# Kernel tuning notes

Measured on AMD Instinct MI355X. Metric: run time of the kernel, lower is better.

## Reference

```python
import jax, jax.numpy as jnp
import numpy as np

N_NODES, N_EDGES, HID = 30000, 480000, 128
N_GRAPHS, N_CLASSES = 128, 6
BN_EPS, ADD_SCORE = 1e-5, 0.5


def setup_inputs():
    key = jax.random.key(0)
    ks = jax.random.split(key, 12)
    g = lambda i, shape: jax.random.normal(ks[i], shape, jnp.float32) * 0.05
    return dict(
        x=jax.random.normal(ks[0], (N_NODES, HID), jnp.float32),
        edge_index=jax.random.randint(ks[1], (2, N_EDGES), 0, N_NODES, jnp.int32),
        batch=jnp.sort(jax.random.randint(ks[2], (N_NODES,), 0, N_GRAPHS, jnp.int32)),
        Wl=g(3, (6, HID, HID)), bl=jnp.zeros((6, HID), jnp.float32),
        Wr=g(4, (6, HID, HID)),
        gamma=jnp.ones((6, HID), jnp.float32), beta=jnp.zeros((6, HID), jnp.float32),
        Wlin=g(5, (3, HID, 2 * HID)), blin=jnp.zeros((3, HID), jnp.float32),
        Wp=g(6, (3, 2 * HID)), bp=jnp.zeros((3,), jnp.float32),
        Wf1=g(7, (HID, HID)), bf1=jnp.zeros((HID,), jnp.float32),
        Wf2=g(8, (N_CLASSES, HID)), bf2=jnp.zeros((N_CLASSES,), jnp.float32),
    )


def _sage(x, src, dst, emf, Wl_i, bl_i, Wr_i, N):
    # PyG SAGEConv: lin_l(mean_{j->i} x_j) + lin_r(x_i); emf masks dead edges
    msg = x[src] * emf[:, None]                              # [E,H]
    s = jax.ops.segment_sum(msg, dst, num_segments=N)
    c = jax.ops.segment_sum(emf, dst, num_segments=N)
    mean = s / jnp.maximum(c, 1.0)[:, None]
    return mean @ Wl_i.T + bl_i + x @ Wr_i.T


def _bn(x, g, b, nvf):
    # training-mode BatchNorm over valid (non-merged-away) nodes only
    cnt = jnp.maximum(nvf.sum(), 1.0)
    mu = (x * nvf[:, None]).sum(0) / cnt
    var = (((x - mu) ** 2) * nvf[:, None]).sum(0) / cnt
    return g * (x - mu) * jax.lax.rsqrt(var + BN_EPS) + b


def _edge_pool(x, src, dst, emb, nvb, Wp_i, bp_i, N, E):
    h = x.shape[1]
    # raw edge score = Linear(cat(x[src], x[dst]))
    raw = (x @ Wp_i[:h])[src] + (x @ Wp_i[h:])[dst] + bp_i   # [E]
    neg = jnp.finfo(x.dtype).min
    mx = jax.ops.segment_max(jnp.where(emb, raw, neg), dst, num_segments=N)
    z = jnp.where(emb, jnp.exp(jnp.where(emb, raw - mx[dst], 0.0)), 0.0)
    den = jax.ops.segment_sum(z, dst, num_segments=N)
    score = z / jnp.maximum(den, 1e-16)[dst] + ADD_SCORE     # softmax per dst + 0.5

    # greedy edge matching in descending score order (sequential, int-only carry)
    order = jnp.argsort(-jnp.where(emb, jax.lax.stop_gradient(score), -jnp.inf))

    def step(carry, i):
        matched, cluster, chosen = carry
        s, t = src[i], dst[i]
        ok = emb[i] & (~matched[s]) & (~matched[t]) & (s != t)
        rep, oth = jnp.minimum(s, t), jnp.maximum(s, t)
        matched = matched.at[s].set(matched[s] | ok)
        matched = matched.at[t].set(matched[t] | ok)
        cluster = cluster.at[oth].set(jnp.where(ok, rep, cluster[oth]))
        chosen = chosen.at[rep].set(jnp.where(ok, i, chosen[rep]))
        return (matched, cluster, chosen), None

    init = (~nvb, jnp.arange(N, dtype=jnp.int32), jnp.full((N,), -1, jnp.int32))
    (matched, cluster, chosen), _ = jax.lax.scan(step, init, order)

    # merged node = (x_s + x_t) * score(chosen edge); singleton score = 1
    nscore = jnp.where(chosen >= 0, score[jnp.maximum(chosen, 0)], 1.0)
    new_x = jax.ops.segment_sum(x, cluster, num_segments=N) * nscore[:, None]
    nvb2 = nvb & (cluster == jnp.arange(N, dtype=jnp.int32))
    # remap edges to cluster representatives; coalesce duplicates (self-loops kept, as PyG)
    key = jnp.where(emb, cluster[src] * N + cluster[dst], -1)  # N*N < 2**31
    uk = jnp.unique(key, size=E, fill_value=-1)
    emb2 = uk >= 0
    ukc = jnp.maximum(uk, 0)
    return new_x, ukc // N, ukc % N, emb2, nvb2


def reference(x, edge_index, batch, Wl, bl, Wr, gamma, beta, Wlin, blin, Wp, bp, Wf1, bf1, Wf2, bf2):
    N, E = x.shape[0], edge_index.shape[1]
    src, dst = edge_index[0], edge_index[1]
    emb = jnp.ones((E,), bool)   # edge-valid mask (fixed-shape graph coarsening)
    nvb = jnp.ones((N,), bool)   # node-valid mask
    for blk in range(3):
        emf, nvf = emb.astype(x.dtype), nvb.astype(x.dtype)
        i = 2 * blk
        h = _bn(jax.nn.relu(_sage(x, src, dst, emf, Wl[i], bl[i], Wr[i], N)), gamma[i], beta[i], nvf)
        h2 = _bn(jax.nn.relu(_sage(h, src, dst, emf, Wl[i + 1], bl[i + 1], Wr[i + 1], N)), gamma[i + 1], beta[i + 1], nvf)
        x = jnp.concatenate([h2, h], axis=1) @ Wlin[blk].T + blin[blk]  # dropout = identity (eval)
        x, src, dst, emb, nvb = _edge_pool(x, src, dst, emb, nvb, Wp[blk], bp[blk], N, E)
    nvf = nvb.astype(x.dtype)
    sums = jax.ops.segment_sum(x * nvf[:, None], batch, num_segments=N_GRAPHS)
    cnt = jax.ops.segment_sum(nvf, batch, num_segments=N_GRAPHS)
    pooled = sums / jnp.maximum(cnt, 1.0)[:, None]           # global_mean_pool
    hfc = jax.nn.relu(pooled @ Wf1.T + bf1)
    return jax.nn.log_softmax(hfc @ Wf2.T + bf2, axis=1)
```

## Files before the change

### kernel.cpp

```cpp
#include <hip/hip_runtime.h>
#include <stdint.h>

#define NN 30000
#define NE 480000
#define HID 128
#define NG 128
#define NC 6
#define BN_EPS 1e-5f
#define WPB 938
#define SLOTS 4

typedef unsigned int u32;
typedef unsigned long long u64;

__global__ void k_init(const int* __restrict__ ei, int* srcA, int* dstA, int* nvb,
                       int* scal, int* b3, int* i2, float* gbuf) {
  int t = blockIdx.x * 256 + threadIdx.x;
  if (t < NE) { srcA[t] = ei[t]; dstA[t] = ei[NE + t]; }
  if (t < NN) nvb[t] = 1;
  if (t < 2 * NN) { b3[t] = 0; i2[t] = 0; }
  if (t < NG * HID + NG) gbuf[t] = 0.f;
  if (t == 0) { scal[0] = NE; scal[1] = 0; }
}

__global__ void k_csr_count(const int* __restrict__ pE, const int* __restrict__ src,
                            const int* __restrict__ dst, int* __restrict__ cnt,
                            int* __restrict__ icnt, const int* __restrict__ nvb,
                            int* __restrict__ pcnt) {
  int t = blockIdx.x * 256 + threadIdx.x;
  if (t < NN && nvb[t]) atomicAdd(pcnt, 1);
  if (t < *pE) {
    int s = src[t], d = dst[t];
    atomicAdd(&cnt[d], 1);
    if (s != d) { atomicAdd(&icnt[s], 1); atomicAdd(&icnt[d], 1); }
  }
}

__global__ __launch_bounds__(1024) void k_scan2(const int* __restrict__ in0, int* __restrict__ out0,
                                                const int* __restrict__ in1, int* __restrict__ out1) {
  const int* in = blockIdx.x ? in1 : in0;
  int* out = blockIdx.x ? out1 : out0;
  __shared__ int part[1024];
  int t = threadIdx.x;
  int chunk = (NN + 1023) / 1024;
  int b = t * chunk, e = b + chunk;
  if (b > NN) b = NN;
  if (e > NN) e = NN;
  int s = 0;
  for (int i = b; i < e; i++) s += in[i];
  part[t] = s;
  __syncthreads();
  for (int off = 1; off < 1024; off <<= 1) {
    int v = (t >= off) ? part[t - off] : 0;
    __syncthreads();
    part[t] += v;
    __syncthreads();
  }
  int excl = (t == 0) ? 0 : part[t - 1];
  for (int i = b; i < e; i++) { out[i] = excl; excl += in[i]; }
  if (t == 0) out[NN] = part[1023];
}

__global__ void k_csr_scatter(const int* __restrict__ pE, const int* __restrict__ src,
                              const int* __restrict__ dst, const int* __restrict__ coff,
                              int* __restrict__ cursor, int* __restrict__ eids,
                              const int* __restrict__ ioff, int* __restrict__ icur,
                              int* __restrict__ ieids) {
  int e = blockIdx.x * 256 + threadIdx.x;
  if (e >= *pE) return;
  int s = src[e], d = dst[e];
  int pos = coff[d] + atomicAdd(&cursor[d], 1);
  eids[pos] = e;
  if (s != d) {
    int p1 = ioff[s] + atomicAdd(&icur[s], 1); ieids[p1] = e;
    int p2 = ioff[d] + atomicAdd(&icur[d], 1); ieids[p2] = e;
  }
}

__global__ __launch_bounds__(256) void k_sage_gather(
    const int* __restrict__ coff, const int* __restrict__ eids,
    const int* __restrict__ src, const float* __restrict__ x,
    float* __restrict__ mean) {
  int grp = threadIdx.x >> 5;
  int lane = threadIdx.x & 31;
  int n = blockIdx.x * 8 + grp;
  if (n >= NN) return;
  int b = coff[n], e2 = coff[n + 1];
  float4 acc = make_float4(0.f, 0.f, 0.f, 0.f);
  for (int i = b; i < e2; i++) {
    int s = src[eids[i]];
    float4 v = *(const float4*)(x + (size_t)s * HID + lane * 4);
    acc.x += v.x; acc.y += v.y; acc.z += v.z; acc.w += v.w;
  }
  float inv = 1.0f / fmaxf((float)(e2 - b), 1.0f);
  acc.x *= inv; acc.y *= inv; acc.z *= inv; acc.w *= inv;
  *(float4*)(mean + (size_t)n * HID + lane * 4) = acc;
}

__global__ __launch_bounds__(256) void gemm_dual(
    const float* __restrict__ A1, const float* __restrict__ W1,
    const float* __restrict__ A2, const float* __restrict__ W2,
    const float* __restrict__ bias, float* __restrict__ out,
    int M, int ldw, int relu, double* __restrict__ bnsum) {
  if (blockIdx.x == 0 && threadIdx.x < 2 * HID) bnsum[threadIdx.x] = 0.0;
  __shared__ float As[64][33];
  __shared__ float Ws[32][132];
  int row0 = blockIdx.x * 64;
  int tid = threadIdx.x;
  int cid = tid & 31;
  int rid = tid >> 5;
  float acc[8][4];
#pragma unroll
  for (int r = 0; r < 8; r++)
#pragma unroll
    for (int c = 0; c < 4; c++) acc[r][c] = 0.f;

  for (int srcI = 0; srcI < 2; ++srcI) {
    const float* A = srcI ? A2 : A1;
    const float* W = srcI ? W2 : W1;
    for (int kc = 0; kc < 128; kc += 32) {
#pragma unroll
      for (int i = 0; i < 2; ++i) {
        int idx = tid + i * 256;
        int r = idx >> 3;
        int c4 = (idx & 7) << 2;
        int gr = row0 + r;
        float4 v = make_float4(0.f, 0.f, 0.f, 0.f);
        if (gr < M) v = *(const float4*)(A + (size_t)gr * 128 + kc + c4);
        As[r][c4 + 0] = v.x; As[r][c4 + 1] = v.y; As[r][c4 + 2] = v.z; As[r][c4 + 3] = v.w;
      }
#pragma unroll
      for (int i = 0; i < 4; ++i) {
        int idx = tid + i * 256;
        int j = idx >> 3;
        int c4 = (idx & 7) << 2;
        float4 v = *(const float4*)(W + (size_t)j * ldw + kc + c4);
        Ws[c4 + 0][j] = v.x; Ws[c4 + 1][j] = v.y; Ws[c4 + 2][j] = v.z; Ws[c4 + 3][j] = v.w;
      }
      __syncthreads();
#pragma unroll
      for (int kk = 0; kk < 32; ++kk) {
        float4 w = *(const float4*)(&Ws[kk][cid * 4]);
#pragma unroll
        for (int r = 0; r < 8; ++r) {
          float a = As[rid * 8 + r][kk];
          acc[r][0] += a * w.x; acc[r][1] += a * w.y; acc[r][2] += a * w.z; acc[r][3] += a * w.w;
        }
      }
      __syncthreads();
    }
  }
#pragma unroll
  for (int r = 0; r < 8; ++r) {
    int gr = row0 + rid * 8 + r;
    if (gr >= M) continue;
#pragma unroll
    for (int c = 0; c < 4; ++c) {
      float v = acc[r][c] + bias[cid * 4 + c];
      if (relu) v = fmaxf(v, 0.f);
      out[(size_t)gr * 128 + cid * 4 + c] = v;
    }
  }
}

__global__ __launch_bounds__(128) void k_bn_stats(const float* __restrict__ x,
                                                  const int* __restrict__ nvb,
                                                  double* __restrict__ sums) {
  int k = threadIdx.x;
  int n0 = blockIdx.x * 64;
  float s = 0.f, q = 0.f;
  for (int r = 0; r < 64; r++) {
    int n = n0 + r;
    if (n >= NN) break;
    if (!nvb[n]) continue;
    float v = x[(size_t)n * HID + k];
    s += v; q += v * v;
  }
  atomicAdd(&sums[k], (double)s);
  atomicAdd(&sums[HID + k], (double)q);
}

__global__ void k_bn_apply(float* __restrict__ x, const double* __restrict__ sums,
                           const int* __restrict__ cnt, const float* __restrict__ gamma,
                           const float* __restrict__ beta) {
  int t = blockIdx.x * 256 + threadIdx.x;
  if (t >= NN * HID) return;
  int k = t & 127;
  double c = (double)((*cnt > 1) ? *cnt : 1);
  double mu = sums[k] / c;
  double var = sums[HID + k] / c - mu * mu;
  if (var < 0.0) var = 0.0;
  float inv = (float)(1.0 / sqrt(var + (double)BN_EPS));
  x[t] = gamma[k] * (x[t] - (float)mu) * inv + beta[k];
}

__global__ void k_node_proj(const float* __restrict__ x, const float* __restrict__ Wp,
                            float* __restrict__ px1, float* __restrict__ px2) {
  int n = blockIdx.x * 256 + threadIdx.x;
  if (n >= NN) return;
  const float* xr = x + (size_t)n * HID;
  float s1 = 0.f, s2 = 0.f;
#pragma unroll 8
  for (int k = 0; k < HID; k += 4) {
    float4 v = *(const float4*)(xr + k);
    float4 w1 = *(const float4*)(Wp + k);
    float4 w2 = *(const float4*)(Wp + HID + k);
    s1 += v.x * w1.x + v.y * w1.y + v.z * w1.z + v.w * w1.w;
    s2 += v.x * w2.x + v.y * w2.y + v.z * w2.z + v.w * w2.w;
  }
  px1[n] = s1; px2[n] = s2;
}

__global__ void k_edge_softmax_seed(
    const int* __restrict__ coff, const int* __restrict__ eids,
    const int* __restrict__ src, const float* __restrict__ px1,
    const float* __restrict__ px2, const float* __restrict__ bp,
    float* __restrict__ score, u64* __restrict__ ekey, u64* __restrict__ S) {
  int n = blockIdx.x * 256 + threadIdx.x;
  if (n >= NN) return;
  S[n] = 0ull;
  int b = coff[n], e2 = coff[n + 1];
  if (b == e2) return;
  float p2 = px2[n] + *bp;
  float mx = -3.4e38f;
  for (int i = b; i < e2; i++) {
    float r = px1[src[eids[i]]] + p2;
    mx = fmaxf(mx, r);
  }
  double den = 0.0;
  for (int i = b; i < e2; i++) {
    int eid = eids[i];
    float z = expf(px1[src[eid]] + p2 - mx);
    score[eid] = z;
    den += (double)z;
  }
  if (den < 1e-16) den = 1e-16;
  double invd = 1.0 / den;
  for (int i = b; i < e2; i++) {
    int eid = eids[i];
    float sc = (float)((double)score[eid] * invd) + 0.5f;
    score[eid] = sc;
    ekey[eid] = ((u64)__float_as_uint(sc) << 32) | (u64)(0xFFFFFFFFu - (u32)eid);
  }
}

__global__ __launch_bounds__(256) void k_suitor(
    const int* __restrict__ ioff, const int* __restrict__ ieids,
    const int* __restrict__ src, const int* __restrict__ dst,
    const u64* __restrict__ ekey, u64* __restrict__ S) {
  int wid = threadIdx.x >> 6;
  int lane = threadIdx.x & 63;
  int n = blockIdx.x * 4 + wid;
  if (n >= NN) return;
  int cur = n;
  while (cur >= 0) {
    int b = ioff[cur], e2 = ioff[cur + 1];
    int deg = e2 - b;
    if (deg == 0) break;
    if (deg <= 64 * SLOTS) {
      u64 key[SLOTS]; int pv[SLOTS];
#pragma unroll
      for (int s = 0; s < SLOTS; s++) {
        key[s] = 0; pv[s] = 0;
        int i = b + s * 64 + lane;
        if (i < e2) {
          int e = ieids[i];
          key[s] = ekey[e];
          int es = src[e], ed = dst[e];
          pv[s] = (es == cur) ? ed : es;
        }
      }
      long long res;
      for (;;) {
        u64 localBest = 0;
#pragma unroll
        for (int s = 0; s < SLOTS; s++) {
          if (!key[s]) continue;
          u64 sv = __hip_atomic_load(&S[pv[s]], __ATOMIC_RELAXED, __HIP_MEMORY_SCOPE_AGENT);
          if (sv >= key[s]) key[s] = 0;
          else if (key[s] > localBest) localBest = key[s];
        }
        u64 bestKey = localBest;
#pragma unroll
        for (int o = 32; o > 0; o >>= 1) {
          u64 other = __shfl_xor(bestKey, o, 64);
          if (other > bestKey) bestKey = other;
        }
        if (bestKey == 0) { res = -1; break; }
        int ms = -1;
#pragma unroll
        for (int s = 0; s < SLOTS; s++)
          if (ms < 0 && key[s] == bestKey) ms = s;
        u64 ball = __ballot(ms >= 0);
        int owner = (int)(__ffsll((long long)ball) - 1);
        long long r0 = -3;
        if (lane == owner) {
          int bv = pv[ms];
          u64 old = atomicMax(&S[bv], bestKey);
          if (old >= bestKey) { key[ms] = 0; r0 = -2; }
          else if (old == 0) r0 = -1;
          else {
            int eo = (int)(0xFFFFFFFFu - (u32)(old & 0xFFFFFFFFull));
            int so = src[eo], do_ = dst[eo];
            r0 = (so == bv) ? do_ : so;
          }
        }
        res = __shfl(r0, owner, 64);
        if (res != -2) break;
      }
      if (res < 0) break;
      cur = (int)res;
    } else {
      u64 bestKey = 0;
      for (int i = b + lane; i < e2; i += 64) {
        int e = ieids[i];
        u64 k = ekey[e];
        if (k <= bestKey) continue;
        int es = src[e], ed = dst[e];
        int v = (es == cur) ? ed : es;
        u64 sv = __hip_atomic_load(&S[v], __ATOMIC_RELAXED, __HIP_MEMORY_SCOPE_AGENT);
        if (k > sv) bestKey = k;
      }
#pragma unroll
      for (int o = 32; o > 0; o >>= 1) {
        u64 other = __shfl_xor(bestKey, o, 64);
        if (other > bestKey) bestKey = other;
      }
      long long r0 = -1;
      if (bestKey != 0 && lane == 0) {
        int e = (int)(0xFFFFFFFFu - (u32)(bestKey & 0xFFFFFFFFull));
        int es = src[e], ed = dst[e];
        int bv = (es == cur) ? ed : es;
        u64 old = atomicMax(&S[bv], bestKey);
        if (old >= bestKey) r0 = cur;
        else if (old != 0) {
          int eo = (int)(0xFFFFFFFFu - (u32)(old & 0xFFFFFFFFull));
          int so = src[eo], do_ = dst[eo];
          r0 = (so == bv) ? do_ : so;
        }
      }
      long long res = (bestKey != 0) ? __shfl(r0, 0, 64) : -1;
      cur = (int)res;
    }
  }
}

__global__ __launch_bounds__(256) void k_new_x(
    const u64* __restrict__ S, const int* __restrict__ src, const int* __restrict__ dst,
    const float* __restrict__ score, const float* __restrict__ x,
    float* __restrict__ out, int* __restrict__ cluster,
    int* __restrict__ nvb, int* __restrict__ b3zero) {
  int gt = blockIdx.x * 256 + threadIdx.x;
  if (gt < 2 * NN) b3zero[gt] = 0;
  int grp = threadIdx.x >> 5;
  int lane = threadIdx.x & 31;
  int n = blockIdx.x * 8 + grp;
  if (n >= NN) return;
  u64 k = S[n];
  int partner = -1;
  bool isOth = false;
  float sc = 1.f;
  if (k) {
    int e = (int)(0xFFFFFFFFu - (u32)(k & 0xFFFFFFFFull));
    int s = src[e], d = dst[e];
    int other = (s == n) ? d : s;
    if (S[other] == k) {
      if (n > other) isOth = true;
      else { partner = other; sc = score[e]; }
    }
  }
  float4 v = make_float4(0.f, 0.f, 0.f, 0.f);
  if (!isOth) {
    v = *(const float4*)(x + (size_t)n * HID + lane * 4);
    if (partner >= 0) {
      float4 w = *(const float4*)(x + (size_t)partner * HID + lane * 4);
      v.x = (v.x + w.x) * sc; v.y = (v.y + w.y) * sc;
      v.z = (v.z + w.z) * sc; v.w = (v.w + w.w) * sc;
    }
  }
  *(float4*)(out + (size_t)n * HID + lane * 4) = v;
  if (lane == 0) {
    int e2 = (int)(0xFFFFFFFFu - (u32)(k & 0xFFFFFFFFull));
    int s2 = isOth ? src[e2] : n;
    int d2 = isOth ? dst[e2] : n;
    cluster[n] = isOth ? (s2 < d2 ? s2 : d2) : n;
    nvb[n] = (nvb[n] && !isOth) ? 1 : 0;
  }
}

__global__ void k_bucket_count(const int* __restrict__ pE, const int* __restrict__ src,
                               const int* __restrict__ cluster, int* __restrict__ bcount) {
  int e = blockIdx.x * 256 + threadIdx.x;
  if (e >= *pE) return;
  atomicAdd(&bcount[cluster[src[e]]], 1);
}

__global__ __launch_bounds__(1024) void k_scan(const int* __restrict__ in, int* __restrict__ out,
                                               int n, int* totalDst) {
  __shared__ int part[1024];
  int t = threadIdx.x;
  int chunk = (n + 1023) / 1024;
  int b = t * chunk, e = b + chunk;
  if (b > n) b = n;
  if (e > n) e = n;
  int s = 0;
  for (int i = b; i < e; i++) s += in[i];
  part[t] = s;
  __syncthreads();
  for (int off = 1; off < 1024; off <<= 1) {
    int v = (t >= off) ? part[t - off] : 0;
    __syncthreads();
    part[t] += v;
    __syncthreads();
  }
  int excl = (t == 0) ? 0 : part[t - 1];
  int total = part[1023];
  for (int i = b; i < e; i++) { out[i] = excl; excl += in[i]; }
  if (t == 0) {
    out[n] = total;
    if (totalDst) *totalDst = total;
  }
}

__global__ void k_bucket_scatter(const int* __restrict__ pE, const int* __restrict__ src,
                                 const int* __restrict__ dst, const int* __restrict__ cluster,
                                 const int* __restrict__ boffs, int* __restrict__ bcursor,
                                 int* __restrict__ bucket) {
  int e = blockIdx.x * 256 + threadIdx.x;
  if (e >= *pE) return;
  int cs = cluster[src[e]], cd = cluster[dst[e]];
  int pos = boffs[cs] + atomicAdd(&bcursor[cs], 1);
  bucket[pos] = cd;
}

__global__ __launch_bounds__(256) void k_dedup_bitmap(
    const int* __restrict__ boffs, int* __restrict__ bucket,
    int* __restrict__ ucount) {
  __shared__ u32 bm[4][960];
  int wid = threadIdx.x >> 6;
  int lane = threadIdx.x & 63;
  int n = blockIdx.x * 4 + wid;
  int b = boffs[n], e = boffs[n + 1];
  for (int w = lane; w < 960; w += 64) bm[wid][w] = 0;
  __syncthreads();
  for (int i = b + lane; i < e; i += 64)
    atomicOr(&bm[wid][bucket[i] >> 5], 1u << (bucket[i] & 31));
  __syncthreads();
  int w0 = lane * 15;
  int w1 = w0 + 15; if (w1 > WPB) w1 = WPB;
  int cnt = 0;
  for (int w = w0; w < w1; w++) cnt += __popc(bm[wid][w]);
  int inc = cnt;
  for (int o = 1; o < 64; o <<= 1) { int v = __shfl_up(inc, o); if (lane >= o) inc += v; }
  int excl = inc - cnt;
  int total = __shfl(inc, 63);
  int pos = b + excl;
  for (int w = w0; w < w1; w++) {
    u32 v = bm[wid][w];
    while (v) { int bit = __ffs(v) - 1; bucket[pos++] = (w << 5) | bit; v &= v - 1; }
  }
  if (lane == 0) ucount[n] = total;
}

__global__ void k_emit(const int* __restrict__ boffs, const int* __restrict__ bucket,
                       const int* __restrict__ bucount, const int* __restrict__ bnoffs,
                       int* __restrict__ srcO, int* __restrict__ dstO,
                       int* __restrict__ b3zero, int* __restrict__ i2zero,
                       int* __restrict__ pcnt) {
  int t = blockIdx.x * 256 + threadIdx.x;
  int stride = gridDim.x * 256;
  for (int z = t; z < 2 * NN; z += stride) { b3zero[z] = 0; i2zero[z] = 0; }
  if (t == 0) *pcnt = 0;
  if (t >= NN) return;
  int u = bucount[t], b = boffs[t], o = bnoffs[t];
  for (int i = 0; i < u; i++) { srcO[o + i] = t; dstO[o + i] = bucket[b + i]; }
}

__global__ void k_graph_pool(const int* __restrict__ nvb, const int* __restrict__ batch,
                             const float* __restrict__ x, float* __restrict__ gsum,
                             float* __restrict__ gcnt) {
  int t = blockIdx.x * 256 + threadIdx.x;
  int n = t >> 2;
  if (n >= NN) return;
  if (!nvb[n]) return;
  int sub = t & 3;
  int g = batch[n];
  const float* xr = x + (size_t)n * HID + sub * 32;
  float* o = gsum + (size_t)g * HID + sub * 32;
#pragma unroll
  for (int i = 0; i < 8; i++) {
    float4 v = *(const float4*)(xr + i * 4);
    atomicAdd(o + i * 4 + 0, v.x); atomicAdd(o + i * 4 + 1, v.y);
    atomicAdd(o + i * 4 + 2, v.z); atomicAdd(o + i * 4 + 3, v.w);
  }
  if (sub == 0) atomicAdd(&gcnt[g], 1.0f);
}

__global__ __launch_bounds__(128) void k_head1(const float* __restrict__ gsum,
                                               const float* __restrict__ gcnt,
                                               const float* __restrict__ Wf1,
                                               const float* __restrict__ bf1,
                                               float* __restrict__ hfc) {
  int g = blockIdx.x;
  int j = threadIdx.x;
  __shared__ float p[HID];
  float c = fmaxf(gcnt[g], 1.f);
  p[j] = gsum[g * HID + j] / c;
  __syncthreads();
  float s = bf1[j];
  const float* w = Wf1 + (size_t)j * HID;
  for (int k = 0; k < HID; k++) s += p[k] * w[k];
  hfc[g * HID + j] = fmaxf(s, 0.f);
}

__global__ void k_head2(const float* __restrict__ hfc, const float* __restrict__ Wf2,
                        const float* __restrict__ bf2, float* __restrict__ out) {
  int g = blockIdx.x;
  int t = threadIdx.x;
  __shared__ float lg[NC];
  if (t < NC) {
    float s = bf2[t];
    const float* w = Wf2 + (size_t)t * HID;
    const float* h = hfc + (size_t)g * HID;
    for (int k = 0; k < HID; k++) s += h[k] * w[k];
    lg[t] = s;
  }
  __syncthreads();
  if (t == 0) {
    float m = lg[0];
    for (int c = 1; c < NC; c++) m = fmaxf(m, lg[c]);
    float se = 0.f;
    for (int c = 0; c < NC; c++) se += expf(lg[c] - m);
    float lse = m + logf(se);
    for (int c = 0; c < NC; c++) out[g * NC + c] = lg[c] - lse;
  }
}

extern "C" void kernel_launch(void* const* d_in, const int* in_sizes, int n_in,
                              void* d_out, int out_size, void* d_ws, size_t ws_size,
                              hipStream_t stream) {
  const float* x0 = (const float*)d_in[0];
  const int* ei = (const int*)d_in[1];
  const int* batch = (const int*)d_in[2];
  const float* Wl = (const float*)d_in[3];
  const float* bl = (const float*)d_in[4];
  const float* Wr = (const float*)d_in[5];
  const float* gamma = (const float*)d_in[6];
  const float* beta = (const float*)d_in[7];
  const float* Wlin = (const float*)d_in[8];
  const float* blin = (const float*)d_in[9];
  const float* Wp = (const float*)d_in[10];
  const float* bp = (const float*)d_in[11];
  const float* Wf1 = (const float*)d_in[12];
  const float* bf1 = (const float*)d_in[13];
  const float* Wf2 = (const float*)d_in[14];
  const float* bf2 = (const float*)d_in[15];
  float* out = (float*)d_out;

  const int NH = NN * HID;
  size_t off = 0;
  char* base = (char*)d_ws;
  auto carve = [&](size_t bytes) -> char* {
    char* p = base + off;
    off += (bytes + 255) & ~(size_t)255;
    return p;
  };
  float* xa = (float*)carve((size_t)NH * 4);
  float* xb = (float*)carve((size_t)NH * 4);
  float* xc = (float*)carve((size_t)NH * 4);
  float* xd = (float*)carve((size_t)NH * 4);
  int* srcA = (int*)carve((size_t)NE * 4);
  int* dstA = (int*)carve((size_t)NE * 4);
  int* srcB = (int*)carve((size_t)NE * 4);
  int* dstB = (int*)carve((size_t)NE * 4);
  float* escore = (float*)carve((size_t)NE * 4);
  int* ebucket = (int*)carve((size_t)NE * 4);
  int* eids = (int*)carve((size_t)NE * 4);
  u64* ekey = (u64*)carve((size_t)NE * 8);
  int* ieids = (int*)carve((size_t)2 * NE * 4);
  u64* S = (u64*)carve((size_t)NN * 8);
  float* npx1 = (float*)carve((size_t)NN * 4);
  float* npx2 = (float*)carve((size_t)NN * 4);
  int* ncluster = (int*)carve((size_t)NN * 4);
  int* nvb = (int*)carve((size_t)NN * 4);
  int* b3 = (int*)carve((size_t)3 * NN * 4);
  int* bcount = b3;
  int* bcursor = b3 + NN;
  int* bucount = b3 + 2 * NN;
  int* i2 = (int*)carve((size_t)2 * NN * 4);
  int* icnt = i2;
  int* icursor = i2 + NN;
  int* boffs = (int*)carve((size_t)(NN + 1) * 4);
  int* bnoffs = (int*)carve((size_t)(NN + 1) * 4);
  int* csroff = (int*)carve((size_t)(NN + 1) * 4);
  int* ioff = (int*)carve((size_t)(NN + 1) * 4);
  double* bnsum = (double*)carve((size_t)2 * HID * 8);
  float* gbuf = (float*)carve((size_t)(NG * HID + NG) * 4);
  float* gsum = gbuf;
  float* gcnt = gbuf + NG * HID;
  float* ghfc = (float*)carve((size_t)NG * HID * 4);
  int* scal = (int*)carve(64 * 4);
  (void)ws_size; (void)n_in; (void)in_sizes; (void)out_size;

  int* pE = scal;
  int* pcnt = scal + 1;

  hipMemcpyAsync(xa, x0, (size_t)NH * 4, hipMemcpyDeviceToDevice, stream);
  k_init<<<1875, 256, 0, stream>>>(ei, srcA, dstA, nvb, scal, b3, i2, gbuf);

  int* srcC = srcA; int* dstC = dstA; int* srcN = srcB; int* dstN = dstB;
  float* xcur = xa;
  float* xtmp = xd;

  auto sage = [&](const float* xin, float* xout, int L) {
    k_sage_gather<<<3750, 256, 0, stream>>>(csroff, eids, srcC, xin, xtmp);
    gemm_dual<<<469, 256, 0, stream>>>(xtmp, Wl + (size_t)L * HID * HID, xin,
                                       Wr + (size_t)L * HID * HID, bl + (size_t)L * HID,
                                       xout, NN, HID, 1, bnsum);
    k_bn_stats<<<469, 128, 0, stream>>>(xout, nvb, bnsum);
    k_bn_apply<<<15000, 256, 0, stream>>>(xout, bnsum, pcnt, gamma + (size_t)L * HID,
                                          beta + (size_t)L * HID);
  };

  for (int b = 0; b < 3; b++) {
    k_csr_count<<<1875, 256, 0, stream>>>(pE, srcC, dstC, bcount, icnt, nvb, pcnt);
    k_scan2<<<2, 1024, 0, stream>>>(bcount, csroff, icnt, ioff);
    k_csr_scatter<<<1875, 256, 0, stream>>>(pE, srcC, dstC, csroff, bcursor, eids,
                                            ioff, icursor, ieids);

    sage(xcur, xb, 2 * b);
    sage(xb, xc, 2 * b + 1);
    gemm_dual<<<469, 256, 0, stream>>>(xc, Wlin + (size_t)b * HID * 2 * HID, xb,
                                       Wlin + (size_t)b * HID * 2 * HID + HID,
                                       blin + (size_t)b * HID, xcur, NN, 2 * HID, 0, bnsum);

    k_node_proj<<<118, 256, 0, stream>>>(xcur, Wp + (size_t)b * 2 * HID, npx1, npx2);
    k_edge_softmax_seed<<<118, 256, 0, stream>>>(csroff, eids, srcC, npx1, npx2, bp + b,
                                                 escore, ekey, S);
    k_suitor<<<7500, 256, 0, stream>>>(ioff, ieids, srcC, dstC, ekey, S);
    k_new_x<<<3750, 256, 0, stream>>>(S, srcC, dstC, escore, xcur, xtmp,
                                      ncluster, nvb, b3);

    if (b < 2) {
      k_bucket_count<<<1875, 256, 0, stream>>>(pE, srcC, ncluster, bcount);
      k_scan<<<1, 1024, 0, stream>>>(bcount, boffs, NN, (int*)nullptr);
      k_bucket_scatter<<<1875, 256, 0, stream>>>(pE, srcC, dstC, ncluster, boffs, bcursor,
                                                 ebucket);
      k_dedup_bitmap<<<7500, 256, 0, stream>>>(boffs, ebucket, bucount);
      k_scan<<<1, 1024, 0, stream>>>(bucount, bnoffs, NN, pE);
      k_emit<<<235, 256, 0, stream>>>(boffs, ebucket, bucount, bnoffs, srcN, dstN,
                                      b3, i2, pcnt);
      { int* t = srcC; srcC = srcN; srcN = t; t = dstC; dstC = dstN; dstN = t; }
    }
    { float* t = xcur; xcur = xtmp; xtmp = t; }
  }

  k_graph_pool<<<469, 256, 0, stream>>>(nvb, batch, xcur, gsum, gcnt);
  k_head1<<<NG, 128, 0, stream>>>(gsum, gcnt, Wf1, bf1, ghfc);
  k_head2<<<NG, 32, 0, stream>>>(ghfc, Wf2, bf2, out);
}
```

Measured before the change: 3.008 ms.

## Pack incidence lists with key and neighbor for suitor matching

Instead of storing edge ids in the incidence list and chasing ekey/src/dst through indirection in the suitor loop, a new scatter kernel runs after scoring and writes int4 entries holding the 64-bit key and the neighbor id. The suitor kernel then reads one contiguous 16-byte entry per incident edge, which removes the dependent random gathers from its inner loop. The list reuses the xc buffer as scratch, which is free at that point. It costs an extra kernel launch and larger per-entry writes. k_new_x also takes the cluster id directly from the partner, dropping a redundant edge lookup.

```diff
diff --git a/kernel.cpp b/kernel.cpp
--- a/kernel.cpp
+++ b/kernel.cpp
@@ -12,6 +12,10 @@
 
 typedef unsigned int u32;
 typedef unsigned long long u64;
+
+__device__ __forceinline__ u64 ent_key(int4 ent) {
+  return ((u64)(u32)ent.y << 32) | (u32)ent.x;
+}
 
 __global__ void k_init(const int* __restrict__ ei, int* srcA, int* dstA, int* nvb,
                        int* scal, int* b3, int* i2, float* gbuf) {
@@ -61,20 +65,14 @@
   if (t == 0) out[NN] = part[1023];
 }
 
-__global__ void k_csr_scatter(const int* __restrict__ pE, const int* __restrict__ src,
-                              const int* __restrict__ dst, const int* __restrict__ coff,
-                              int* __restrict__ cursor, int* __restrict__ eids,
-                              const int* __restrict__ ioff, int* __restrict__ icur,
-                              int* __restrict__ ieids) {
+__global__ void k_csr_scatter(const int* __restrict__ pE, const int* __restrict__ dst,
+                              const int* __restrict__ coff, int* __restrict__ cursor,
+                              int* __restrict__ eids) {
   int e = blockIdx.x * 256 + threadIdx.x;
   if (e >= *pE) return;
-  int s = src[e], d = dst[e];
+  int d = dst[e];
   int pos = coff[d] + atomicAdd(&cursor[d], 1);
   eids[pos] = e;
-  if (s != d) {
-    int p1 = ioff[s] + atomicAdd(&icur[s], 1); ieids[p1] = e;
-    int p2 = ioff[d] + atomicAdd(&icur[d], 1); ieids[p2] = e;
-  }
 }
 
 __global__ __launch_bounds__(256) void k_sage_gather(
@@ -244,10 +242,29 @@
   }
 }
 
+__global__ void k_inc_scatter(const int* __restrict__ pE, const int* __restrict__ src,
+                              const int* __restrict__ dst, const u64* __restrict__ ekey,
+                              const int* __restrict__ ioff, int* __restrict__ icur,
+                              int4* __restrict__ ielist) {
+  int e = blockIdx.x * 256 + threadIdx.x;
+  if (e >= *pE) return;
+  int s = src[e], d = dst[e];
+  if (s == d) return;
+  u64 k = ekey[e];
+  int4 ent;
+  ent.x = (int)(u32)(k & 0xFFFFFFFFull);
+  ent.y = (int)(u32)(k >> 32);
+  ent.w = 0;
+  ent.z = d;
+  ielist[ioff[s] + atomicAdd(&icur[s], 1)] = ent;
+  ent.z = s;
+  ielist[ioff[d] + atomicAdd(&icur[d], 1)] = ent;
+}
+
 __global__ __launch_bounds__(256) void k_suitor(
-    const int* __restrict__ ioff, const int* __restrict__ ieids,
+    const int* __restrict__ ioff, const int4* __restrict__ ielist,
     const int* __restrict__ src, const int* __restrict__ dst,
-    const u64* __restrict__ ekey, u64* __restrict__ S) {
+    u64* __restrict__ S) {
   int wid = threadIdx.x >> 6;
   int lane = threadIdx.x & 63;
   int n = blockIdx.x * 4 + wid;
@@ -264,10 +281,9 @@
         key[s] = 0; pv[s] = 0;
         int i = b + s * 64 + lane;
         if (i < e2) {
-          int e = ieids[i];
-          key[s] = ekey[e];
-          int es = src[e], ed = dst[e];
-          pv[s] = (es == cur) ? ed : es;
+          int4 ent = ielist[i];
+          key[s] = ent_key(ent);
+          pv[s] = ent.z;
         }
       }
       long long res;
@@ -313,12 +329,10 @@
     } else {
       u64 bestKey = 0;
       for (int i = b + lane; i < e2; i += 64) {
-        int e = ieids[i];
-        u64 k = ekey[e];
+        int4 ent = ielist[i];
+        u64 k = ent_key(ent);
         if (k <= bestKey) continue;
-        int es = src[e], ed = dst[e];
-        int v = (es == cur) ? ed : es;
-        u64 sv = __hip_atomic_load(&S[v], __ATOMIC_RELAXED, __HIP_MEMORY_SCOPE_AGENT);
+        u64 sv = __hip_atomic_load(&S[ent.z], __ATOMIC_RELAXED, __HIP_MEMORY_SCOPE_AGENT);
         if (k > sv) bestKey = k;
       }
 #pragma unroll
@@ -358,6 +372,7 @@
   if (n >= NN) return;
   u64 k = S[n];
   int partner = -1;
+  int rep = n;
   bool isOth = false;
   float sc = 1.f;
   if (k) {
@@ -365,7 +380,7 @@
     int s = src[e], d = dst[e];
     int other = (s == n) ? d : s;
     if (S[other] == k) {
-      if (n > other) isOth = true;
+      if (n > other) { isOth = true; rep = other; }
       else { partner = other; sc = score[e]; }
     }
   }
@@ -380,10 +395,7 @@
   }
   *(float4*)(out + (size_t)n * HID + lane * 4) = v;
   if (lane == 0) {
-    int e2 = (int)(0xFFFFFFFFu - (u32)(k & 0xFFFFFFFFull));
-    int s2 = isOth ? src[e2] : n;
-    int d2 = isOth ? dst[e2] : n;
-    cluster[n] = isOth ? (s2 < d2 ? s2 : d2) : n;
+    cluster[n] = rep;
     nvb[n] = (nvb[n] && !isOth) ? 1 : 0;
   }
 }
@@ -577,7 +589,6 @@
   int* ebucket = (int*)carve((size_t)NE * 4);
   int* eids = (int*)carve((size_t)NE * 4);
   u64* ekey = (u64*)carve((size_t)NE * 8);
-  int* ieids = (int*)carve((size_t)2 * NE * 4);
   u64* S = (u64*)carve((size_t)NN * 8);
   float* npx1 = (float*)carve((size_t)NN * 4);
   float* npx2 = (float*)carve((size_t)NN * 4);
@@ -602,6 +613,8 @@
   int* scal = (int*)carve(64 * 4);
   (void)ws_size; (void)n_in; (void)in_sizes; (void)out_size;
 
+  int4* ielist = (int4*)xc;
+
   int* pE = scal;
   int* pcnt = scal + 1;
 
@@ -625,8 +638,7 @@
   for (int b = 0; b < 3; b++) {
     k_csr_count<<<1875, 256, 0, stream>>>(pE, srcC, dstC, bcount, icnt, nvb, pcnt);
     k_scan2<<<2, 1024, 0, stream>>>(bcount, csroff, icnt, ioff);
-    k_csr_scatter<<<1875, 256, 0, stream>>>(pE, srcC, dstC, csroff, bcursor, eids,
-                                            ioff, icursor, ieids);
+    k_csr_scatter<<<1875, 256, 0, stream>>>(pE, dstC, csroff, bcursor, eids);
 
     sage(xcur, xb, 2 * b);
     sage(xb, xc, 2 * b + 1);
@@ -637,7 +649,8 @@
     k_node_proj<<<118, 256, 0, stream>>>(xcur, Wp + (size_t)b * 2 * HID, npx1, npx2);
     k_edge_softmax_seed<<<118, 256, 0, stream>>>(csroff, eids, srcC, npx1, npx2, bp + b,
                                                  escore, ekey, S);
-    k_suitor<<<7500, 256, 0, stream>>>(ioff, ieids, srcC, dstC, ekey, S);
+    k_inc_scatter<<<1875, 256, 0, stream>>>(pE, srcC, dstC, ekey, ioff, icursor, ielist);
+    k_suitor<<<7500, 256, 0, stream>>>(ioff, ielist, srcC, dstC, S);
     k_new_x<<<3750, 256, 0, stream>>>(S, srcC, dstC, escore, xcur, xtmp,
                                       ncluster, nvb, b3);
 
```

Measured after the change: 2.843 ms. 1.06x faster.
